# Kernel tuning notes

Measured on AMD Instinct MI355X. Metric: run time of the kernel, lower is better.

Reference implementation:

```python
import jax, jax.numpy as jnp
import numpy as np

N, E, L, D = 4, 64, 512, 256


def setup_inputs() -> dict:
    key = jax.random.key(0)
    k1, k2, k3 = jax.random.split(key, 3)
    doc_state = jax.random.normal(k1, (N, L, D), dtype=jnp.float32)
    nodes_mapping = (jax.random.uniform(k2, (N, E, L)) < 0.1).astype(jnp.float32)
    # entity lengths = number of selected tokens (some may be 0, exercising the guard)
    nodes_len = jnp.sum(nodes_mapping, axis=2)  # N x E, float32
    return {"doc_state": doc_state, "nodes_mapping": nodes_mapping, "nodes_len": nodes_len}


def reference(doc_state, nodes_mapping, nodes_len):
    # entity_states: N x E x L x d = mask-broadcast of token states
    entity_states = nodes_mapping[:, :, :, None] * doc_state[:, None, :, :]
    max_pooled = jnp.max(entity_states, axis=2)          # N x E x d
    safe_len = jnp.where(nodes_len > 0, nodes_len, jnp.ones_like(nodes_len))
    mean_pooled = jnp.sum(entity_states, axis=2) / safe_len[:, :, None]  # N x E x d
    return jnp.concatenate([max_pooled, mean_pooled], axis=2)  # N x E x 2d
```

## Files before the change

### kernel.cpp

```cpp
#include <hip/hip_runtime.h>
#include <math.h>

#define PN 4
#define PE 64
#define PL 512
#define PD 256
#define NWAVES 16
#define TOK_PER_WAVE (PL / NWAVES)

__global__ __launch_bounds__(64 * NWAVES) void MeanMaxPooling_84473416778475_kernel(
    const float* __restrict__ doc_state,
    const float* __restrict__ nodes_mapping,
    const float* __restrict__ nodes_len,
    float* __restrict__ out)
{
    const int ne   = blockIdx.x;
    const int n    = ne >> 6;
    const int e    = ne & 63;
    const int tid  = threadIdx.x;
    const int w    = tid >> 6;
    const int lane = tid & 63;

    __shared__ float  smask[PL];
    __shared__ float4 s_sum[NWAVES][64];
    __shared__ float4 s_max[NWAVES][64];

    if (tid < PL) {
        smask[tid] = nodes_mapping[(size_t)(n * PE + e) * PL + tid];
    }
    __syncthreads();

    const float4* ds = (const float4*)(doc_state + (size_t)n * PL * PD);

    float4 sum = make_float4(0.f, 0.f, 0.f, 0.f);
    float4 mx  = make_float4(-INFINITY, -INFINITY, -INFINITY, -INFINITY);

    const int l0 = w * TOK_PER_WAVE;
    #pragma unroll 8
    for (int i = 0; i < TOK_PER_WAVE; ++i) {
        const int l = l0 + i;
        const float  m = smask[l];
        const float4 s = ds[l * 64 + lane];
        const float vx = m * s.x, vy = m * s.y, vz = m * s.z, vw = m * s.w;
        sum.x += vx; sum.y += vy; sum.z += vz; sum.w += vw;
        mx.x = fmaxf(mx.x, vx);
        mx.y = fmaxf(mx.y, vy);
        mx.z = fmaxf(mx.z, vz);
        mx.w = fmaxf(mx.w, vw);
    }

    s_sum[w][lane] = sum;
    s_max[w][lane] = mx;
    __syncthreads();

    if (tid < 64) {
        float4 tsum = s_sum[0][lane];
        float4 tmax = s_max[0][lane];
        #pragma unroll
        for (int j = 1; j < NWAVES; ++j) {
            const float4 s2 = s_sum[j][lane];
            const float4 m2 = s_max[j][lane];
            tsum.x += s2.x; tsum.y += s2.y; tsum.z += s2.z; tsum.w += s2.w;
            tmax.x = fmaxf(tmax.x, m2.x);
            tmax.y = fmaxf(tmax.y, m2.y);
            tmax.z = fmaxf(tmax.z, m2.z);
            tmax.w = fmaxf(tmax.w, m2.w);
        }
        const float len  = nodes_len[n * PE + e];
        const float slen = (len > 0.f) ? len : 1.0f;
        float4 mean;
        mean.x = tsum.x / slen;
        mean.y = tsum.y / slen;
        mean.z = tsum.z / slen;
        mean.w = tsum.w / slen;

        float4* o = (float4*)(out + (size_t)(n * PE + e) * 2 * PD);
        o[lane]      = tmax;
        o[64 + lane] = mean;
    }
}

extern "C" void kernel_launch(void* const* d_in, const int* in_sizes, int n_in,
                              void* d_out, int out_size, void* d_ws, size_t ws_size,
                              hipStream_t stream) {
    const float* doc_state     = (const float*)d_in[0];
    const float* nodes_mapping = (const float*)d_in[1];
    const float* nodes_len     = (const float*)d_in[2];
    float* out = (float*)d_out;

    dim3 grid(PN * PE);
    dim3 block(64 * NWAVES);
    MeanMaxPooling_84473416778475_kernel<<<grid, block, 0, stream>>>(
        doc_state, nodes_mapping, nodes_len, out);
}
```

Measured before the change: 63.34 us.

## Split pooling into token-chunk partials with entity grouping plus combine kernel

Replaces the single per-entity kernel with a two-stage scheme. The first kernel processes four entities per block over a 32-token chunk, so each doc_state load is reused across four entities, and it writes per-chunk max and sum partials to workspace. A second kernel reduces the 16 chunks per entity and applies the mean division. This cuts redundant doc_state reads and uses smaller blocks. In exchange it adds a second launch and a round trip through global memory for the partials, and it depends on the workspace being large enough.

```diff
diff --git a/kernel.cpp b/kernel.cpp
--- a/kernel.cpp
+++ b/kernel.cpp
@@ -5,79 +5,124 @@
 #define PE 64
 #define PL 512
 #define PD 256
-#define NWAVES 16
-#define TOK_PER_WAVE (PL / NWAVES)
+#define GC 16
+#define TOK_PER_CHUNK (PL / GC)
+#define EG 4
+#define NEG (PE / EG)
+#define D4 (PD / 4)
 
-__global__ __launch_bounds__(64 * NWAVES) void MeanMaxPooling_84473416778475_kernel(
+__global__ __launch_bounds__(256) void mmp_partial(
     const float* __restrict__ doc_state,
     const float* __restrict__ nodes_mapping,
+    float* __restrict__ part)
+{
+    const int bx = blockIdx.x;
+    const int c  = bx & (GC - 1);
+    const int eg = (bx >> 4) & (NEG - 1);
+    const int n  = bx >> 8;
+
+    const int tid  = threadIdx.x;
+    const int w    = tid >> 6;
+    const int lane = tid & 63;
+
+    __shared__ float  smask[EG][TOK_PER_CHUNK];
+    __shared__ float4 s_sum[4][EG][D4];
+    __shared__ float4 s_max[4][EG][D4];
+
+    if (tid < EG * TOK_PER_CHUNK) {
+        const int j = tid >> 5;
+        const int t = tid & 31;
+        smask[j][t] = nodes_mapping[(size_t)(n * PE + eg * EG + j) * PL
+                                    + c * TOK_PER_CHUNK + t];
+    }
+    __syncthreads();
+
+    const float4* ds = (const float4*)(doc_state + (size_t)n * PL * PD);
+    const float4* dsp = ds + (size_t)(c * TOK_PER_CHUNK + w * 8) * D4 + lane;
+
+    float4 sum[EG], mx[EG];
+    #pragma unroll
+    for (int j = 0; j < EG; ++j) {
+        sum[j] = make_float4(0.f, 0.f, 0.f, 0.f);
+        mx[j]  = make_float4(-INFINITY, -INFINITY, -INFINITY, -INFINITY);
+    }
+
+    #pragma unroll
+    for (int i = 0; i < 8; ++i) {
+        const float4 s = dsp[i * D4];
+        #pragma unroll
+        for (int j = 0; j < EG; ++j) {
+            const float m = smask[j][w * 8 + i];
+            const float vx = m * s.x, vy = m * s.y, vz = m * s.z, vw = m * s.w;
+            sum[j].x += vx; sum[j].y += vy; sum[j].z += vz; sum[j].w += vw;
+            mx[j].x = fmaxf(mx[j].x, vx);
+            mx[j].y = fmaxf(mx[j].y, vy);
+            mx[j].z = fmaxf(mx[j].z, vz);
+            mx[j].w = fmaxf(mx[j].w, vw);
+        }
+    }
+
+    #pragma unroll
+    for (int j = 0; j < EG; ++j) {
+        s_sum[w][j][lane] = sum[j];
+        s_max[w][j][lane] = mx[j];
+    }
+    __syncthreads();
+
+    {
+        const int j = tid >> 6;
+        float4 tm = s_max[0][j][lane];
+        float4 ts = s_sum[0][j][lane];
+        #pragma unroll
+        for (int w2 = 1; w2 < 4; ++w2) {
+            const float4 m2 = s_max[w2][j][lane];
+            const float4 s2 = s_sum[w2][j][lane];
+            tm.x = fmaxf(tm.x, m2.x); tm.y = fmaxf(tm.y, m2.y);
+            tm.z = fmaxf(tm.z, m2.z); tm.w = fmaxf(tm.w, m2.w);
+            ts.x += s2.x; ts.y += s2.y; ts.z += s2.z; ts.w += s2.w;
+        }
+        float4* p = (float4*)part;
+        const size_t e    = (size_t)(n * PE + eg * EG + j);
+        const size_t base = ((e * GC + c) * 2) * D4;
+        p[base + lane]      = tm;
+        p[base + D4 + lane] = ts;
+    }
+}
+
+__global__ __launch_bounds__(128) void mmp_combine(
+    const float* __restrict__ part,
     const float* __restrict__ nodes_len,
     float* __restrict__ out)
 {
     const int ne   = blockIdx.x;
-    const int n    = ne >> 6;
-    const int e    = ne & 63;
     const int tid  = threadIdx.x;
-    const int w    = tid >> 6;
+    const int k    = tid >> 6;
     const int lane = tid & 63;
 
-    __shared__ float  smask[PL];
-    __shared__ float4 s_sum[NWAVES][64];
-    __shared__ float4 s_max[NWAVES][64];
+    const float4* p = (const float4*)part;
+    const size_t base = (((size_t)ne * GC) * 2 + k) * D4 + lane;
 
-    if (tid < PL) {
-        smask[tid] = nodes_mapping[(size_t)(n * PE + e) * PL + tid];
-    }
-    __syncthreads();
-
-    const float4* ds = (const float4*)(doc_state + (size_t)n * PL * PD);
-
-    float4 sum = make_float4(0.f, 0.f, 0.f, 0.f);
-    float4 mx  = make_float4(-INFINITY, -INFINITY, -INFINITY, -INFINITY);
-
-    const int l0 = w * TOK_PER_WAVE;
-    #pragma unroll 8
-    for (int i = 0; i < TOK_PER_WAVE; ++i) {
-        const int l = l0 + i;
-        const float  m = smask[l];
-        const float4 s = ds[l * 64 + lane];
-        const float vx = m * s.x, vy = m * s.y, vz = m * s.z, vw = m * s.w;
-        sum.x += vx; sum.y += vy; sum.z += vz; sum.w += vw;
-        mx.x = fmaxf(mx.x, vx);
-        mx.y = fmaxf(mx.y, vy);
-        mx.z = fmaxf(mx.z, vz);
-        mx.w = fmaxf(mx.w, vw);
+    float4 acc = p[base];
+    if (k == 0) {
+        #pragma unroll
+        for (int c = 1; c < GC; ++c) {
+            const float4 v = p[base + (size_t)c * 2 * D4];
+            acc.x = fmaxf(acc.x, v.x); acc.y = fmaxf(acc.y, v.y);
+            acc.z = fmaxf(acc.z, v.z); acc.w = fmaxf(acc.w, v.w);
+        }
+    } else {
+        #pragma unroll
+        for (int c = 1; c < GC; ++c) {
+            const float4 v = p[base + (size_t)c * 2 * D4];
+            acc.x += v.x; acc.y += v.y; acc.z += v.z; acc.w += v.w;
+        }
+        const float len  = nodes_len[ne];
+        const float slen = (len > 0.f) ? len : 1.0f;
+        acc.x /= slen; acc.y /= slen; acc.z /= slen; acc.w /= slen;
     }
 
-    s_sum[w][lane] = sum;
-    s_max[w][lane] = mx;
-    __syncthreads();
-
-    if (tid < 64) {
-        float4 tsum = s_sum[0][lane];
-        float4 tmax = s_max[0][lane];
-        #pragma unroll
-        for (int j = 1; j < NWAVES; ++j) {
-            const float4 s2 = s_sum[j][lane];
-            const float4 m2 = s_max[j][lane];
-            tsum.x += s2.x; tsum.y += s2.y; tsum.z += s2.z; tsum.w += s2.w;
-            tmax.x = fmaxf(tmax.x, m2.x);
-            tmax.y = fmaxf(tmax.y, m2.y);
-            tmax.z = fmaxf(tmax.z, m2.z);
-            tmax.w = fmaxf(tmax.w, m2.w);
-        }
-        const float len  = nodes_len[n * PE + e];
-        const float slen = (len > 0.f) ? len : 1.0f;
-        float4 mean;
-        mean.x = tsum.x / slen;
-        mean.y = tsum.y / slen;
-        mean.z = tsum.z / slen;
-        mean.w = tsum.w / slen;
-
-        float4* o = (float4*)(out + (size_t)(n * PE + e) * 2 * PD);
-        o[lane]      = tmax;
-        o[64 + lane] = mean;
-    }
+    float4* o = (float4*)out;
+    o[(size_t)ne * 2 * D4 + k * D4 + lane] = acc;
 }
 
 extern "C" void kernel_launch(void* const* d_in, const int* in_sizes, int n_in,
@@ -86,10 +131,11 @@
     const float* doc_state     = (const float*)d_in[0];
     const float* nodes_mapping = (const float*)d_in[1];
     const float* nodes_len     = (const float*)d_in[2];
-    float* out = (float*)d_out;
+    float* out  = (float*)d_out;
+    float* part = (float*)d_ws;
 
-    dim3 grid(PN * PE);
-    dim3 block(64 * NWAVES);
-    MeanMaxPooling_84473416778475_kernel<<<grid, block, 0, stream>>>(
-        doc_state, nodes_mapping, nodes_len, out);
+    mmp_partial<<<dim3(PN * NEG * GC), dim3(256), 0, stream>>>(
+        doc_state, nodes_mapping, part);
+    mmp_combine<<<dim3(PN * PE), dim3(128), 0, stream>>>(
+        part, nodes_len, out);
 }
```

Result: slower. 65.04 us (+2.7%).
